# Kernel tuning notes

Hardware: AMD Instinct MI355X
Metric: run time of the kernel (lower is better)

## Reference

```python
import jax, jax.numpy as jnp
import numpy as np
from jax import lax

FP = 64   # frame side
DP = 28   # digit template side
CP = FP - DP + 1  # 37, valid correlation output side


def setup_inputs() -> dict:
    key = jax.random.key(0)
    ks = jax.random.split(key, 6)
    B, T, S, H = 128, 16, 10, 256
    frames = jax.random.normal(ks[0], (B, T, FP, FP), dtype=jnp.float32)
    digit_images = jax.random.uniform(ks[1], (S, B, DP, DP), dtype=jnp.float32)
    W1 = jax.random.normal(ks[2], (CP * CP, H), dtype=jnp.float32) * (1.0 / np.sqrt(CP * CP))
    b1 = jnp.zeros((H,), dtype=jnp.float32)
    W2 = jax.random.normal(ks[3], (H, 2), dtype=jnp.float32) * (1.0 / np.sqrt(H))
    b2 = jnp.zeros((2,), dtype=jnp.float32)
    where_std = jnp.ones((2,), dtype=jnp.float32) * 0.1
    return {"frames": frames, "digit_images": digit_images, "S": S,
            "W1": W1, "b1": b1, "W2": W2, "b2": b2, "where_std": where_std}


def reference(frames, digit_images, S, W1, b1, W2, b2, where_std):
    B, T = frames.shape[0], frames.shape[1]
    # torch: conv2d(frames.transpose(0,1), digit_images.view(S*B,DP,DP).unsqueeze(1), groups=B)
    # lhs: (T, B, FP, FP) treated as batch=T, channels=B; rhs: (S*B, 1, DP, DP)
    lhs = jnp.transpose(frames, (1, 0, 2, 3))              # (T, B, FP, FP)
    rhs = digit_images.reshape(S * B, 1, DP, DP)           # (S*B, 1, DP, DP)
    convolved = lax.conv_general_dilated(
        lhs, rhs, window_strides=(1, 1), padding='VALID',
        feature_group_count=B,
        dimension_numbers=('NCHW', 'OIHW', 'NCHW'))        # (T, S*B, CP, CP)
    convolved = convolved.reshape(T, S, B, CP * CP)
    hidden = jnp.tanh(convolved @ W1 + b1)                 # (T, S, B, H)
    q_mean = jnp.tanh(hidden @ W2 + b2)                    # (T, S, B, 2)
    q_mean = jnp.transpose(q_mean, (1, 2, 0, 3))           # (S, B, T, 2)
    eps = jax.random.normal(jax.random.key(1), q_mean.shape, dtype=q_mean.dtype)
    z_where = q_mean + where_std * eps                     # Normal(q_mean, std).sample()
    return q_mean, z_where
```

## Files before the change

kernel.cpp:

```cpp
#include <hip/hip_runtime.h>
#include <stdint.h>

#define CROWB 2816
#define NOUT 40960

typedef _Float16 f16x8 __attribute__((ext_vector_type(8)));
typedef float f32x4 __attribute__((ext_vector_type(4)));

#define TF_ROT(x, r) (((x) << (r)) | ((x) >> (32 - (r))))
#define TF_ROUND(r) { x0 += x1; x1 = TF_ROT(x1, (r)); x1 ^= x0; }

__device__ __forceinline__ float erfinv_f(float x) {
  float w = -log1pf(-x * x);
  float p;
  if (w < 5.0f) {
    w -= 2.5f;
    p = 2.81022636e-08f;
    p = fmaf(p, w, 3.43273939e-07f);
    p = fmaf(p, w, -3.5233877e-06f);
    p = fmaf(p, w, -4.39150654e-06f);
    p = fmaf(p, w, 0.00021858087f);
    p = fmaf(p, w, -0.00125372503f);
    p = fmaf(p, w, -0.00417768164f);
    p = fmaf(p, w, 0.246640727f);
    p = fmaf(p, w, 1.50140941f);
  } else {
    w = sqrtf(w) - 3.0f;
    p = -0.000200214257f;
    p = fmaf(p, w, 0.000100950558f);
    p = fmaf(p, w, 0.00134934322f);
    p = fmaf(p, w, -0.00367342844f);
    p = fmaf(p, w, 0.00573950773f);
    p = fmaf(p, w, -0.0076224613f);
    p = fmaf(p, w, 0.00943887047f);
    p = fmaf(p, w, 1.00167406f);
    p = fmaf(p, w, 2.83297682f);
  }
  return p * x;
}

__device__ __forceinline__ float gauss_eps(int p) {
  const unsigned ks0 = 0u, ks1 = 1u, ks2 = 0x1BD11BDBu;
  unsigned x0 = 0u + ks0;
  unsigned x1 = (unsigned)p + ks1;
  TF_ROUND(13) TF_ROUND(15) TF_ROUND(26) TF_ROUND(6)
  x0 += ks1; x1 += ks2 + 1u;
  TF_ROUND(17) TF_ROUND(29) TF_ROUND(16) TF_ROUND(24)
  x0 += ks2; x1 += ks0 + 2u;
  TF_ROUND(13) TF_ROUND(15) TF_ROUND(26) TF_ROUND(6)
  x0 += ks0; x1 += ks1 + 3u;
  TF_ROUND(17) TF_ROUND(29) TF_ROUND(16) TF_ROUND(24)
  x0 += ks1; x1 += ks2 + 4u;
  TF_ROUND(13) TF_ROUND(15) TF_ROUND(26) TF_ROUND(6)
  x0 += ks2; x1 += ks0 + 5u;
  unsigned bits = x0 ^ x1;
  unsigned fb = (bits >> 9) | 0x3f800000u;
  float f = __uint_as_float(fb) - 1.0f;
  const float lo = -0.99999994f;
  float u = f * 2.0f + lo;
  u = fmaxf(lo, u);
  return 1.41421356f * erfinv_f(u);
}

__device__ __forceinline__ float fast_tanh(float x) {
  float e = __expf(2.0f * x);
  return 1.0f - 2.0f * __builtin_amdgcn_rcpf(e + 1.0f);
}

__device__ __forceinline__ uint32_t packh2(float lo, float hi) {
  union { _Float16 h[2]; uint32_t u; } c;
  c.h[0] = (_Float16)lo; c.h[1] = (_Float16)hi;
  return c.u;
}

__global__ void prep_w1t(const float* __restrict__ W1, uint8_t* __restrict__ w1t) {
  int k = blockIdx.x;
  int h = threadIdx.x;
  float v = (k < 1369) ? W1[(size_t)k * 256 + h] : 0.0f;
  *(_Float16*)(w1t + (size_t)h * CROWB + (size_t)k * 2) = (_Float16)v;
}

__global__ __launch_bounds__(256, 3) void conv_mfma(
    const float* __restrict__ frames, const float* __restrict__ digits,
    uint8_t* __restrict__ conv_out)
{
  __shared__ __align__(16) uint8_t smem[45312];
  const int g = blockIdx.x >> 4, t = blockIdx.x & 15;
  const int tid = threadIdx.x;
  const int lane = tid & 63, w = tid >> 6;
  const int l15 = lane & 15, lg = lane >> 4;
  const int jo = lg * 8;

  {
    const float* fbase = frames + ((size_t)(g * 16 + t)) * 4096;
    float f[16];
    const float4* f4 = (const float4*)(fbase + tid * 16);
    #pragma unroll
    for (int a = 0; a < 4; ++a) {
      float4 v = f4[a];
      f[4*a] = v.x; f[4*a+1] = v.y; f[4*a+2] = v.z; f[4*a+3] = v.w;
    }
    float nxt = __shfl_down(f[0], 1);
    if ((tid & 63) == 63) nxt = (tid == 255) ? 0.0f : fbase[tid * 16 + 16];
    uint32_t we[8], wo[8];
    #pragma unroll
    for (int a = 0; a < 8; ++a) {
      we[a] = packh2(f[2*a], f[2*a+1]);
      float hi = (a == 7) ? nxt : f[2*a+2];
      wo[a] = packh2(f[2*a+1], hi);
    }
    *(uint4*)(smem + tid * 32)          = make_uint4(we[0], we[1], we[2], we[3]);
    *(uint4*)(smem + tid * 32 + 16)     = make_uint4(we[4], we[5], we[6], we[7]);
    *(uint4*)(smem + 8192 + tid * 32)   = make_uint4(wo[0], wo[1], wo[2], wo[3]);
    *(uint4*)(smem + 8192 + tid * 32 + 16) = make_uint4(wo[4], wo[5], wo[6], wo[7]);
  }
  {
    uint32_t* dz = (uint32_t*)(smem + 16384);
    for (int q = tid; q < 7232; q += 256) dz[q] = 0u;
  }
  __syncthreads();
  {
    const float* dsrc = digits + (size_t)g * 7840;
    for (int idx = tid; idx < 7840; idx += 256) {
      int s = idx / 784; int r = idx - s * 784;
      int i = r / 28;    int j = r - i * 28;
      *(_Float16*)(smem + 16384 + (size_t)(s * 904 + i * 32 + j) * 2) = (_Float16)dsrc[idx];
    }
  }
  __syncthreads();

  uint32_t addr0[22];
  #pragma unroll
  for (int j2 = 0; j2 < 22; ++j2) {
    int tile = w + 4 * j2;
    int p = tile * 16 + l15;
    int py = p / 37, px = p - py * 37;
    int a0 = py * 64 + px + jo;
    addr0[j2] = ((uint32_t)(a0 & ~1) << 1) + ((uint32_t)(a0 & 1) << 13);
  }

  f32x4 acc[22];
  #pragma unroll
  for (int j2 = 0; j2 < 22; ++j2) acc[j2] = (f32x4){0.f, 0.f, 0.f, 0.f};

  const uint8_t* dghb = smem + 16384;
  for (int i = 0; i < 28; ++i) {
    f16x8 bfrag = *(const f16x8*)(dghb + (size_t)(l15 * 904 + i * 32 + jo) * 2);
    #pragma unroll
    for (int j2 = 0; j2 < 22; ++j2) {
      const uint32_t* ap = (const uint32_t*)(smem + addr0[j2] + i * 128);
      union { uint32_t u[4]; f16x8 v; } A;
      A.u[0] = ap[0]; A.u[1] = ap[1]; A.u[2] = ap[2]; A.u[3] = ap[3];
      acc[j2] = __builtin_amdgcn_mfma_f32_16x16x32_f16(A.v, bfrag, acc[j2], 0, 0, 0);
    }
  }

  if (l15 < 10) {
    size_t rb = ((size_t)t * 1280 + 10 * g + l15) * (size_t)CROWB;
    #pragma unroll
    for (int j2 = 0; j2 < 22; ++j2) {
      int p0 = (w + 4 * j2) * 16 + lg * 4;
      #pragma unroll
      for (int r = 0; r < 4; ++r) {
        int p = p0 + r;
        if (p < 1369)
          *(_Float16*)(conv_out + rb + (size_t)p * 2) = (_Float16)acc[j2][r];
      }
    }
  }
}

__global__ __launch_bounds__(256) void mlp_mfma(
    const uint8_t* __restrict__ conv_out, const uint8_t* __restrict__ w1t,
    const float* __restrict__ b1, const float* __restrict__ W2,
    const float* __restrict__ b2, const float* __restrict__ wstd,
    float* __restrict__ out)
{
  __shared__ __align__(16) uint8_t smem[43008];
  const int tid = threadIdx.x;
  const int lane = tid & 63, w = tid >> 6;
  const int l15 = lane & 15, lg = lane >> 4;
  const int m0 = blockIdx.x * 64;

  f32x4 acc[4][4];
  #pragma unroll
  for (int mt = 0; mt < 4; ++mt)
    #pragma unroll
    for (int nj = 0; nj < 4; ++nj) acc[mt][nj] = (f32x4){0.f, 0.f, 0.f, 0.f};

  for (int k0 = 0; k0 < 1408; k0 += 64) {
    __syncthreads();
    #pragma unroll
    for (int it = 0; it < 2; ++it) {
      int q = tid + 256 * it; int R = q >> 3, c16 = q & 7;
      uint4 v = *(const uint4*)(conv_out + (size_t)(m0 + R) * CROWB + (size_t)k0 * 2 + c16 * 16);
      *(uint4*)(smem + R * 128 + ((c16 * 16) ^ ((R & 7) << 4))) = v;
    }
    #pragma unroll
    for (int it = 0; it < 8; ++it) {
      int q = tid + 256 * it; int h = q >> 3, c16 = q & 7;
      uint4 v = *(const uint4*)(w1t + (size_t)h * CROWB + (size_t)k0 * 2 + c16 * 16);
      *(uint4*)(smem + 8192 + h * 128 + ((c16 * 16) ^ ((h & 7) << 4))) = v;
    }
    __syncthreads();
    #pragma unroll
    for (int q = 0; q < 2; ++q) {
      f16x8 bf[4];
      #pragma unroll
      for (int nj = 0; nj < 4; ++nj) {
        int h = (w * 4 + nj) * 16 + l15;
        bf[nj] = *(const f16x8*)(smem + 8192 + h * 128 + ((q * 64 + lg * 16) ^ ((h & 7) << 4)));
      }
      #pragma unroll
      for (int mt = 0; mt < 4; ++mt) {
        int R = mt * 16 + l15;
        union { uint4 u; f16x8 v; } A;
        A.u = *(const uint4*)(smem + R * 128 + ((q * 64 + lg * 16) ^ ((R & 7) << 4)));
        #pragma unroll
        for (int nj = 0; nj < 4; ++nj)
          acc[mt][nj] = __builtin_amdgcn_mfma_f32_16x16x32_f16(A.v, bf[nj], acc[mt][nj], 0, 0, 0);
      }
    }
  }

  float qp[4][4][2];
  #pragma unroll
  for (int mt = 0; mt < 4; ++mt)
    #pragma unroll
    for (int r = 0; r < 4; ++r) { qp[mt][r][0] = 0.f; qp[mt][r][1] = 0.f; }

  #pragma unroll
  for (int nj = 0; nj < 4; ++nj) {
    int h = (w * 4 + nj) * 16 + l15;
    float bb = b1[h];
    float w20 = W2[2 * h], w21 = W2[2 * h + 1];
    #pragma unroll
    for (int mt = 0; mt < 4; ++mt)
      #pragma unroll
      for (int r = 0; r < 4; ++r) {
        float hid = fast_tanh(acc[mt][nj][r] + bb);
        qp[mt][r][0] = fmaf(hid, w20, qp[mt][r][0]);
        qp[mt][r][1] = fmaf(hid, w21, qp[mt][r][1]);
      }
  }
  #pragma unroll
  for (int off = 1; off <= 8; off <<= 1) {
    #pragma unroll
    for (int mt = 0; mt < 4; ++mt)
      #pragma unroll
      for (int r = 0; r < 4; ++r) {
        qp[mt][r][0] += __shfl_xor(qp[mt][r][0], off);
        qp[mt][r][1] += __shfl_xor(qp[mt][r][1], off);
      }
  }
  float* qb = (float*)(smem + 40960);
  if (l15 == 0) {
    #pragma unroll
    for (int mt = 0; mt < 4; ++mt)
      #pragma unroll
      for (int r = 0; r < 4; ++r) {
        int row = mt * 16 + lg * 4 + r;
        qb[(w * 64 + row) * 2 + 0] = qp[mt][r][0];
        qb[(w * 64 + row) * 2 + 1] = qp[mt][r][1];
      }
  }
  __syncthreads();
  if (tid < 128) {
    int row = tid >> 1, c = tid & 1;
    float sum = qb[row * 2 + c] + qb[(64 + row) * 2 + c] +
                qb[(128 + row) * 2 + c] + qb[(192 + row) * 2 + c];
    float q = fast_tanh(sum + b2[c]);
    int m = m0 + row;
    int tt = m / 1280;
    int o = m - tt * 1280;
    int base = (o * 16 + tt) * 2;
    out[base + c] = q;
    out[NOUT + base + c] = q + wstd[c] * gauss_eps(base + c);
  }
}

extern "C" void kernel_launch(void* const* d_in, const int* in_sizes, int n_in,
                              void* d_out, int out_size, void* d_ws, size_t ws_size,
                              hipStream_t stream) {
  const float* frames = (const float*)d_in[0];
  const float* digits = (const float*)d_in[1];
  const float* W1   = (const float*)d_in[3];
  const float* b1   = (const float*)d_in[4];
  const float* W2   = (const float*)d_in[5];
  const float* b2   = (const float*)d_in[6];
  const float* wstd = (const float*)d_in[7];
  uint8_t* conv_ws = (uint8_t*)d_ws;
  uint8_t* w1t     = conv_ws + (size_t)20480 * CROWB;
  float* out = (float*)d_out;

  prep_w1t<<<dim3(1408), dim3(256), 0, stream>>>(W1, w1t);
  conv_mfma<<<dim3(2048), dim3(256), 0, stream>>>(frames, digits, conv_ws);
  mlp_mfma<<<dim3(320), dim3(256), 0, stream>>>(conv_ws, w1t, b1, W2, b2, wstd, out);
}
```

Before: 271.8 us.

## Store frame in LDS as overlapping fp16 quads to use 64-bit A-fragment loads

The frame's LDS staging changes from even/odd-shifted fp16 copies to a layout that stores, for every pixel, a 4-element window plus its odd-shifted counterpart, with a rotated chunk order across threads. Each MFMA A fragment is then assembled from two 8-byte loads instead of four 4-byte loads, and the digit template stride is padded to 920 to reduce bank conflicts. The aim is fewer LDS instructions in the inner conv loop. In exchange, LDS use grows to about 62KB and launch bounds drop from 3 to 2 blocks per CU, which reduces occupancy.

```diff
diff --git a/kernel.cpp b/kernel.cpp
--- a/kernel.cpp
+++ b/kernel.cpp
@@ -3,6 +3,8 @@
 
 #define CROWB 2816
 #define NOUT 40960
+#define DGB 32832
+#define DGSTR 920
 
 typedef _Float16 f16x8 __attribute__((ext_vector_type(8)));
 typedef float f32x4 __attribute__((ext_vector_type(4)));
@@ -80,11 +82,11 @@
   *(_Float16*)(w1t + (size_t)h * CROWB + (size_t)k * 2) = (_Float16)v;
 }
 
-__global__ __launch_bounds__(256, 3) void conv_mfma(
+__global__ __launch_bounds__(256, 2) void conv_mfma(
     const float* __restrict__ frames, const float* __restrict__ digits,
     uint8_t* __restrict__ conv_out)
 {
-  __shared__ __align__(16) uint8_t smem[45312];
+  __shared__ __align__(16) uint8_t smem[62272];
   const int g = blockIdx.x >> 4, t = blockIdx.x & 15;
   const int tid = threadIdx.x;
   const int lane = tid & 63, w = tid >> 6;
@@ -93,30 +95,39 @@
 
   {
     const float* fbase = frames + ((size_t)(g * 16 + t)) * 4096;
-    float f[16];
+    float h[20];
     const float4* f4 = (const float4*)(fbase + tid * 16);
     #pragma unroll
     for (int a = 0; a < 4; ++a) {
       float4 v = f4[a];
-      f[4*a] = v.x; f[4*a+1] = v.y; f[4*a+2] = v.z; f[4*a+3] = v.w;
-    }
-    float nxt = __shfl_down(f[0], 1);
-    if ((tid & 63) == 63) nxt = (tid == 255) ? 0.0f : fbase[tid * 16 + 16];
-    uint32_t we[8], wo[8];
-    #pragma unroll
-    for (int a = 0; a < 8; ++a) {
-      we[a] = packh2(f[2*a], f[2*a+1]);
-      float hi = (a == 7) ? nxt : f[2*a+2];
-      wo[a] = packh2(f[2*a+1], hi);
-    }
-    *(uint4*)(smem + tid * 32)          = make_uint4(we[0], we[1], we[2], we[3]);
-    *(uint4*)(smem + tid * 32 + 16)     = make_uint4(we[4], we[5], we[6], we[7]);
-    *(uint4*)(smem + 8192 + tid * 32)   = make_uint4(wo[0], wo[1], wo[2], wo[3]);
-    *(uint4*)(smem + 8192 + tid * 32 + 16) = make_uint4(wo[4], wo[5], wo[6], wo[7]);
+      h[4*a] = v.x; h[4*a+1] = v.y; h[4*a+2] = v.z; h[4*a+3] = v.w;
+    }
+    float t0 = __shfl_down(h[0], 1), t1 = __shfl_down(h[1], 1),
+          t2 = __shfl_down(h[2], 1), t3 = __shfl_down(h[3], 1);
+    if (lane == 63) {
+      int bidx = tid * 16 + 16;
+      t0 = (bidx + 0 < 4096) ? fbase[bidx + 0] : 0.0f;
+      t1 = (bidx + 1 < 4096) ? fbase[bidx + 1] : 0.0f;
+      t2 = (bidx + 2 < 4096) ? fbase[bidx + 2] : 0.0f;
+      t3 = (bidx + 3 < 4096) ? fbase[bidx + 3] : 0.0f;
+    }
+    h[16] = t0; h[17] = t1; h[18] = t2; h[19] = t3;
+    #pragma unroll
+    for (int c = 0; c < 8; ++c) {
+      int cc = (c + tid) & 7;
+      int le = 2 * cc;
+      uint4 v;
+      v.x = packh2(h[le],   h[le+1]);
+      v.y = packh2(h[le+2], h[le+3]);
+      v.z = packh2(h[le+1], h[le+2]);
+      v.w = packh2(h[le+3], h[le+4]);
+      *(uint4*)(smem + 128 * tid + 16 * cc) = v;
+    }
+    if (tid < 16) *(uint32_t*)(smem + 32768 + tid * 4) = 0u;
   }
   {
-    uint32_t* dz = (uint32_t*)(smem + 16384);
-    for (int q = tid; q < 7232; q += 256) dz[q] = 0u;
+    uint32_t* dz = (uint32_t*)(smem + DGB);
+    for (int q = tid; q < 7360; q += 256) dz[q] = 0u;
   }
   __syncthreads();
   {
@@ -124,33 +135,32 @@
     for (int idx = tid; idx < 7840; idx += 256) {
       int s = idx / 784; int r = idx - s * 784;
       int i = r / 28;    int j = r - i * 28;
-      *(_Float16*)(smem + 16384 + (size_t)(s * 904 + i * 32 + j) * 2) = (_Float16)dsrc[idx];
+      *(_Float16*)(smem + DGB + (size_t)(s * DGSTR + i * 32 + j) * 2) = (_Float16)dsrc[idx];
     }
   }
   __syncthreads();
 
-  uint32_t addr0[22];
+  uint32_t abase[22];
   #pragma unroll
   for (int j2 = 0; j2 < 22; ++j2) {
     int tile = w + 4 * j2;
     int p = tile * 16 + l15;
     int py = p / 37, px = p - py * 37;
-    int a0 = py * 64 + px + jo;
-    addr0[j2] = ((uint32_t)(a0 & ~1) << 1) + ((uint32_t)(a0 & 1) << 13);
+    abase[j2] = (uint32_t)(py * 64 + px + jo) * 8u;
   }
 
   f32x4 acc[22];
   #pragma unroll
   for (int j2 = 0; j2 < 22; ++j2) acc[j2] = (f32x4){0.f, 0.f, 0.f, 0.f};
 
-  const uint8_t* dghb = smem + 16384;
   for (int i = 0; i < 28; ++i) {
-    f16x8 bfrag = *(const f16x8*)(dghb + (size_t)(l15 * 904 + i * 32 + jo) * 2);
+    f16x8 bfrag = *(const f16x8*)(smem + DGB + (size_t)(l15 * DGSTR + i * 32 + jo) * 2);
     #pragma unroll
     for (int j2 = 0; j2 < 22; ++j2) {
-      const uint32_t* ap = (const uint32_t*)(smem + addr0[j2] + i * 128);
-      union { uint32_t u[4]; f16x8 v; } A;
-      A.u[0] = ap[0]; A.u[1] = ap[1]; A.u[2] = ap[2]; A.u[3] = ap[3];
+      const uint8_t* ap = smem + abase[j2] + i * 512;
+      union { uint2 u2[2]; f16x8 v; } A;
+      A.u2[0] = *(const uint2*)(ap);
+      A.u2[1] = *(const uint2*)(ap + 32);
       acc[j2] = __builtin_amdgcn_mfma_f32_16x16x32_f16(A.v, bfrag, acc[j2], 0, 0, 0);
     }
   }
```

Result: no change. 268.3 us (-1.3%).
